# Performance work log

Hardware: AMD Instinct MI355X
Metric: run time of the kernel (lower is better)

The kernel has to match this reference:

```python
import jax, jax.numpy as jnp
import numpy as np

H = 16
NUM_LANDMARKS = 32


def setup_inputs() -> dict:
    key = jax.random.key(0)
    ks = jax.random.split(key, 8)
    B, L, D, hd = 2, 2048, 1024, 64
    x = jax.random.normal(ks[0], (B, L, D), dtype=jnp.float32)
    wscale = 1.0 / np.sqrt(D)
    wq = jax.random.normal(ks[1], (D, D), dtype=jnp.float32) * wscale
    wk = jax.random.normal(ks[2], (D, D), dtype=jnp.float32) * wscale
    wv = jax.random.normal(ks[3], (D, D), dtype=jnp.float32) * wscale
    wo = jax.random.normal(ks[4], (D, D), dtype=jnp.float32) * wscale
    memory_gate = jnp.zeros((1,), dtype=jnp.float32)
    memory_decay = jnp.asarray(2.944, dtype=jnp.float32)
    # standard RoPE angle table: theta_j = 10000^(-2j/hd)
    inv_freq = 1.0 / (10000.0 ** (np.arange(0, hd, 2, dtype=np.float32) / hd))
    ang = np.outer(np.arange(L, dtype=np.float32), inv_freq)  # (L, hd//2)
    freqs_cos = jnp.asarray(np.cos(ang), dtype=jnp.float32)
    freqs_sin = jnp.asarray(np.sin(ang), dtype=jnp.float32)
    # previous-chunk memory: phi features are >= 0, Z accumulates ~NUM_LANDMARKS
    M_old = jax.random.normal(ks[5], (B, H, hd, hd), dtype=jnp.float32) * 0.1
    Z_old = jax.random.uniform(ks[6], (B, H, hd), dtype=jnp.float32) * NUM_LANDMARKS + 1.0
    return {"x": x, "wq": wq, "wk": wk, "wv": wv, "wo": wo,
            "memory_gate": memory_gate, "memory_decay": memory_decay,
            "freqs_cos": freqs_cos, "freqs_sin": freqs_sin,
            "M_old": M_old, "Z_old": Z_old}


def reference(x, wq, wk, wv, wo, memory_gate, memory_decay,
              freqs_cos, freqs_sin, M_old, Z_old):
    B, L, D = x.shape
    hd = D // H

    def proj(w):
        # nn.Linear: x @ W^T, then split heads -> (B, H, L, hd)
        return (x @ w.T).reshape(B, L, H, hd).transpose(0, 2, 1, 3)

    q_base, k_base, v = proj(wq), proj(wk), proj(wv)

    def rope(t):
        # complex multiply on adjacent pairs of the head dim
        tr = t.reshape(B, H, L, hd // 2, 2)
        t0, t1 = tr[..., 0], tr[..., 1]
        cos = freqs_cos[None, None]  # (1,1,L,hd//2)
        sin = freqs_sin[None, None]
        o0 = t0 * cos - t1 * sin
        o1 = t0 * sin + t1 * cos
        return jnp.stack([o0, o1], axis=-1).reshape(B, H, L, hd)

    q_rope, k_rope = rope(q_base), rope(k_base)

    # causal SDPA
    scale = 1.0 / jnp.sqrt(jnp.asarray(hd, dtype=q_rope.dtype))
    scores = jnp.einsum('bhqd,bhkd->bhqk', q_rope, k_rope) * scale
    causal = jnp.tril(jnp.ones((L, L), dtype=bool))
    scores = jnp.where(causal[None, None], scores, jnp.finfo(scores.dtype).min)
    attn = jax.nn.softmax(scores, axis=-1)
    local_out = jnp.einsum('bhqk,bhkd->bhqd', attn, v)

    # linear-attention memory read (uses un-rotated q_base)
    phi_Q = jax.nn.elu(q_base) + 1.0
    num = jnp.einsum('bhld,bhde->bhle', phi_Q, M_old)
    den = jnp.sum(phi_Q * Z_old[:, :, None, :], axis=-1, keepdims=True) + 1e-6
    global_out = num / den
    gate = jax.nn.sigmoid(memory_gate)  # (1,)
    out = local_out + gate * global_out

    # landmark compression: adaptive avg pool == uniform chunk means (L % M == 0)
    def landmarks(t):
        return t.reshape(B, H, NUM_LANDMARKS, L // NUM_LANDMARKS, hd).mean(axis=3)

    phi_K = jax.nn.elu(landmarks(k_base)) + 1.0
    landmark_v = landmarks(v)
    delta_M = jnp.einsum('bhmd,bhme->bhde', phi_K, landmark_v)
    delta_Z = phi_K.sum(axis=-2)

    decay = jax.nn.sigmoid(memory_decay)
    M_new = M_old * decay + delta_M
    Z_new = Z_old * decay + delta_Z

    out = out.transpose(0, 2, 1, 3).reshape(B, L, D)
    y = out @ wo.T
    return y, M_new, Z_new
```

## Files before the change

### kernel.cpp

```cpp
#include <hip/hip_runtime.h>
#include <math.h>

#define NH 16
#define HD 64
#define NB 2
#define LSEQ 2048
#define DM 1024
#define NLM 32

#define OUT_M 4194304
#define OUT_Z 4325376

typedef unsigned short u16;
typedef short bf16x8 __attribute__((ext_vector_type(8)));
typedef float f32x16 __attribute__((ext_vector_type(16)));
typedef unsigned short u16x4 __attribute__((ext_vector_type(4)));

__device__ __forceinline__ float sigmoidf_(float x) { return 1.0f / (1.0f + __expf(-x)); }
__device__ __forceinline__ float phif_(float x) { return x > 0.0f ? x + 1.0f : __expf(x); }

__device__ __forceinline__ u16 f2b(float f) {
    union { float f; unsigned u; } v; v.f = f;
    unsigned r = v.u + 0x7FFFu + ((v.u >> 16) & 1u);
    return (u16)(r >> 16);
}
__device__ __forceinline__ float b2f(u16 b) {
    union { unsigned u; float f; } v; v.u = ((unsigned)b) << 16; return v.f;
}
__device__ __forceinline__ int cvtpkbf(float lo, float hi2) {
    int r;
    asm("v_cvt_pk_bf16_f32 %0, %1, %2" : "=v"(r) : "v"(lo), "v"(hi2));
    return r;
}
__device__ __forceinline__ void gload16(const u16* g, u16* l) {
    __builtin_amdgcn_global_load_lds(
        (const __attribute__((address_space(1))) void*)g,
        (__attribute__((address_space(3))) void*)l, 16, 0, 0);
}

__global__ __launch_bounds__(256) void cvt_all(
    const float* __restrict__ x, const float* __restrict__ wq,
    const float* __restrict__ wk, const float* __restrict__ wv,
    const float* __restrict__ wo, u16* __restrict__ dst) {
    size_t i = ((size_t)blockIdx.x * 256 + threadIdx.x) * 8;
    const float* src;
    size_t off;
    if (i < 4194304)      { src = x;  off = i; }
    else if (i < 5242880) { src = wq; off = i - 4194304; }
    else if (i < 6291456) { src = wk; off = i - 5242880; }
    else if (i < 7340032) { src = wv; off = i - 6291456; }
    else                  { src = wo; off = i - 7340032; }
    float4 a = *(const float4*)(src + off);
    float4 b = *(const float4*)(src + off + 4);
    u16 o[8] = {f2b(a.x), f2b(a.y), f2b(a.z), f2b(a.w),
                f2b(b.x), f2b(b.y), f2b(b.z), f2b(b.w)};
    *(int4*)(dst + i) = *(int4*)o;
}

template <int MODE>
__global__ __launch_bounds__(256) void gemm_mfma(
    const u16* __restrict__ A, const u16* __restrict__ W,
    float* __restrict__ Cf, u16* __restrict__ qb, u16* __restrict__ qrp,
    u16* __restrict__ kbp, u16* __restrict__ krp, u16* __restrict__ vbp,
    const float* __restrict__ fcos, const float* __restrict__ fsin) {
    __shared__ u16 As[128 * 64];
    __shared__ u16 Ws[128 * 64];
    const int tid = threadIdx.x;
    const int m0 = blockIdx.x * 128;
    const int n0 = blockIdx.y * 128;
    const int w = tid >> 6;
    const int lane = tid & 63;
    const int l31 = lane & 31;
    const int khalf = lane >> 5;
    const int wr0 = (w >> 1) * 64;
    const int wc0 = (w & 1) * 64;

    const u16* Ag = A + (size_t)m0 * DM;
    const u16* Wg = W + (size_t)n0 * DM;

    const int st_uoff[4] = {w * 4096, w * 4096 + 1024, w * 4096 + 2048, w * 4096 + 3072};
    int st_row[4], st_cc[4];
#pragma unroll
    for (int i = 0; i < 4; ++i) {
        const int off = st_uoff[i] + lane * 16;
        st_row[i] = off >> 7;
        st_cc[i] = ((off >> 4) & 7) ^ (st_row[i] & 7);
    }

    f32x16 acc[2][2];
#pragma unroll
    for (int mf = 0; mf < 2; ++mf)
#pragma unroll
        for (int nf = 0; nf < 2; ++nf)
#pragma unroll
            for (int i = 0; i < 16; ++i) acc[mf][nf][i] = 0.f;

    for (int k0 = 0; k0 < DM; k0 += 64) {
        __syncthreads();
#pragma unroll
        for (int i = 0; i < 4; ++i)
            gload16(Ag + (size_t)st_row[i] * DM + k0 + st_cc[i] * 8,
                    (u16*)((char*)As + st_uoff[i]));
#pragma unroll
        for (int i = 0; i < 4; ++i)
            gload16(Wg + (size_t)st_row[i] * DM + k0 + st_cc[i] * 8,
                    (u16*)((char*)Ws + st_uoff[i]));
        __syncthreads();
#pragma unroll
        for (int ko = 0; ko < 4; ++ko) {
            const int cl = ko * 2 + khalf;
            const int ra0 = wr0 + l31, ra1 = wr0 + 32 + l31;
            const int rb0 = wc0 + l31, rb1 = wc0 + 32 + l31;
            bf16x8 af0 = *(const bf16x8*)((char*)As + ra0 * 128 + ((cl ^ (ra0 & 7)) * 16));
            bf16x8 af1 = *(const bf16x8*)((char*)As + ra1 * 128 + ((cl ^ (ra1 & 7)) * 16));
            bf16x8 bf0 = *(const bf16x8*)((char*)Ws + rb0 * 128 + ((cl ^ (rb0 & 7)) * 16));
            bf16x8 bf1 = *(const bf16x8*)((char*)Ws + rb1 * 128 + ((cl ^ (rb1 & 7)) * 16));
            acc[0][0] = __builtin_amdgcn_mfma_f32_32x32x16_bf16(af0, bf0, acc[0][0], 0, 0, 0);
            acc[0][1] = __builtin_amdgcn_mfma_f32_32x32x16_bf16(af0, bf1, acc[0][1], 0, 0, 0);
            acc[1][0] = __builtin_amdgcn_mfma_f32_32x32x16_bf16(af1, bf0, acc[1][0], 0, 0, 0);
            acc[1][1] = __builtin_amdgcn_mfma_f32_32x32x16_bf16(af1, bf1, acc[1][1], 0, 0, 0);
        }
    }

#pragma unroll
    for (int mf = 0; mf < 2; ++mf) {
#pragma unroll
        for (int nf = 0; nf < 2; ++nf) {
            const int nn = n0 + wc0 + nf * 32 + l31;
#pragma unroll
            for (int reg = 0; reg < 16; ++reg) {
                const int m = m0 + wr0 + mf * 32 + (reg & 3) + 8 * (reg >> 2) + 4 * khalf;
                const float val = acc[mf][nf][reg];
                if (MODE == 1) {
                    Cf[(size_t)m * DM + nn] = val;
                } else {
                    const int b = m >> 11, l = m & (LSEQ - 1);
                    const int mat = nn >> 10;
                    const int n = nn & 1023;
                    const int h = n >> 6, d = n & 63;
                    const size_t hs = (((size_t)(b * NH + h)) * LSEQ + l) * HD + d;
                    const float p = __shfl_xor(val, 1);
                    if (mat == 2) {
                        vbp[hs] = f2b(val);
                    } else {
                        u16* bs = mat ? kbp : qb;
                        u16* rs = mat ? krp : qrp;
                        bs[hs] = f2b(val);
                        const float c = fcos[l * 32 + (d >> 1)];
                        const float s = fsin[l * 32 + (d >> 1)];
                        float o = (d & 1) ? (p * s + val * c) : (val * c - p * s);
                        if (mat == 0) o *= 0.125f;
                        rs[hs] = f2b(o);
                    }
                }
            }
        }
    }
}

__global__ __launch_bounds__(256) void landmarks(
    const u16* __restrict__ kbase, const u16* __restrict__ vbase,
    float* __restrict__ lkq, float* __restrict__ lvq) {
    __shared__ float redk[4][HD];
    __shared__ float redv[4][HD];
    const int bh = blockIdx.x >> 5;
    const int m = blockIdx.x & 31;
    const int tid = threadIdx.x;
    const int ls = tid >> 6;
    const int d = tid & 63;
    const u16* kb = kbase + ((size_t)bh * LSEQ + m * 64) * HD;
    const u16* vb = vbase + ((size_t)bh * LSEQ + m * 64) * HD;
    float sk = 0.f, sv = 0.f;
    for (int l = ls; l < 64; l += 4) {
        sk += b2f(kb[(size_t)l * HD + d]);
        sv += b2f(vb[(size_t)l * HD + d]);
    }
    redk[ls][d] = sk;
    redv[ls][d] = sv;
    __syncthreads();
    if (tid < 64) {
        float mk = (redk[0][d] + redk[1][d] + redk[2][d] + redk[3][d]) * (1.0f / 64.0f);
        float mv = (redv[0][d] + redv[1][d] + redv[2][d] + redv[3][d]) * (1.0f / 64.0f);
        lkq[((size_t)bh * NLM + m) * HD + d] = phif_(mk);
        lvq[((size_t)bh * NLM + m) * HD + d] = mv;
    }
}

__global__ __launch_bounds__(256) void mem_update(
    const float* __restrict__ lkq, const float* __restrict__ lvq,
    const float* __restrict__ M_old, const float* __restrict__ Z_old,
    const float* __restrict__ decay_p, float* __restrict__ out) {
    __shared__ float lk[NLM][HD];
    __shared__ float lv[NLM][HD];
    const int bh = blockIdx.x;
    const int tid = threadIdx.x;
    const float decay = sigmoidf_(decay_p[0]);
#pragma unroll
    for (int i = 0; i < 8; ++i) {
        int idx = tid + 256 * i;
        lk[idx >> 6][idx & 63] = lkq[(size_t)bh * (NLM * HD) + idx];
        lv[idx >> 6][idx & 63] = lvq[(size_t)bh * (NLM * HD) + idx];
    }
    __syncthreads();
    const size_t mo = (size_t)bh * HD * HD;
#pragma unroll
    for (int p = 0; p < 16; ++p) {
        int idx = tid + 256 * p;
        int dd = idx >> 6, e = idx & 63;
        float s = 0.f;
#pragma unroll
        for (int m = 0; m < NLM; ++m) s = fmaf(lk[m][dd], lv[m][e], s);
        out[OUT_M + mo + idx] = M_old[mo + idx] * decay + s;
    }
    if (tid < 64) {
        float s = 0.f;
#pragma unroll
        for (int m = 0; m < NLM; ++m) s += lk[m][tid];
        out[OUT_Z + (size_t)bh * HD + tid] = Z_old[(size_t)bh * HD + tid] * decay + s;
    }
}

__global__ __launch_bounds__(256) void combine(
    const u16* __restrict__ qbase, const float* __restrict__ att,
    const float* __restrict__ M_old, const float* __restrict__ Z_old,
    const float* __restrict__ gate_p, u16* __restrict__ ctxb) {
    __shared__ float phiQ[64][68];
    __shared__ float Ms[64][64];
    __shared__ float Zs[64];
    const int l0 = blockIdx.x * 64;
    const int bh = blockIdx.y;
    const int b = bh >> 4, h = bh & 15;
    const int tid = threadIdx.x;
    const float gate = sigmoidf_(gate_p[0]);

    {
        const int r = tid >> 2, c0 = (tid & 3) << 4;
        const float* Mo = M_old + (size_t)bh * HD * HD + (size_t)r * HD + c0;
#pragma unroll
        for (int i = 0; i < 4; ++i)
            *reinterpret_cast<float4*>(&Ms[r][c0 + 4 * i]) =
                *reinterpret_cast<const float4*>(Mo + 4 * i);
        if (tid < 64) Zs[tid] = Z_old[(size_t)bh * HD + tid];
        const u16* q = qbase + ((size_t)bh * LSEQ + l0 + r) * HD + c0;
#pragma unroll
        for (int i = 0; i < 4; ++i) {
            u16x4 q4 = *(const u16x4*)(q + 4 * i);
            phiQ[r][c0 + 4 * i + 0] = phif_(b2f(q4[0]));
            phiQ[r][c0 + 4 * i + 1] = phif_(b2f(q4[1]));
            phiQ[r][c0 + 4 * i + 2] = phif_(b2f(q4[2]));
            phiQ[r][c0 + 4 * i + 3] = phif_(b2f(q4[3]));
        }
    }
    __syncthreads();

    const int lr = tid >> 2, sub = tid & 3, e0 = sub << 4;
    float den = 0.f;
#pragma unroll
    for (int i = 0; i < 16; ++i) den = fmaf(phiQ[lr][e0 + i], Zs[e0 + i], den);
    den += __shfl_xor(den, 1);
    den += __shfl_xor(den, 2);
    den += 1e-6f;

    float acc[16] = {};
    for (int dd = 0; dd < 64; ++dd) {
        const float pq = phiQ[lr][dd];
#pragma unroll
        for (int i = 0; i < 16; ++i) acc[i] = fmaf(pq, Ms[dd][e0 + i], acc[i]);
    }
    const float g = gate / den;
    const size_t rowoff = ((size_t)b * LSEQ + l0 + lr) * DM + h * HD + e0;
    const float* ap = att + rowoff;
    u16 o[16];
#pragma unroll
    for (int i = 0; i < 4; ++i) {
        float4 a4 = *(const float4*)(ap + 4 * i);
        o[4 * i + 0] = f2b(a4.x + g * acc[4 * i + 0]);
        o[4 * i + 1] = f2b(a4.y + g * acc[4 * i + 1]);
        o[4 * i + 2] = f2b(a4.z + g * acc[4 * i + 2]);
        o[4 * i + 3] = f2b(a4.w + g * acc[4 * i + 3]);
    }
    *(int4*)(ctxb + rowoff) = *(int4*)o;
    *(int4*)(ctxb + rowoff + 8) = *(int4*)(o + 8);
}

__global__ __launch_bounds__(256) void flash_mfma(
    const u16* __restrict__ qr, const u16* __restrict__ kr,
    const u16* __restrict__ vv, float* __restrict__ att) {
    __shared__ int4 smem4[2048];
    char* lds = (char*)smem4;

    const int bid = blockIdx.x;
    const int bx = (bid < 256) ? (15 - (bid >> 5)) : ((bid - 256) >> 5);
    const int bh = bid & 31;
    const int q0 = bx * 128;
    const int tid = threadIdx.x;
    const int w = tid >> 6;
    const int lane = tid & 63;
    const int hi = lane >> 5;
    const int l31 = lane & 31;
    const int qw0 = q0 + w * 32;
    const int tdiag = qw0 >> 6;
    const int nt = 2 * bx + 2;
    const size_t base_bh = (size_t)bh * (LSEQ * HD);

#pragma unroll
    for (int i = 0; i < 4; ++i) {
        int u = tid + 256 * i;
        int row = u >> 3, c = u & 7;
        int4 val = *(const int4*)(qr + base_bh + (size_t)(q0 + row) * HD + c * 8);
        *(int4*)(lds + 16384 + row * 128 + ((c ^ (row & 7)) * 16)) = val;
    }

    int r_[2], c_[2], skoff_[2], svoff_[2];
#pragma unroll
    for (int j = 0; j < 2; ++j) {
        int u = tid + 256 * j;
        int r = u >> 3, c = u & 7;
        r_[j] = r; c_[j] = c;
        skoff_[j] = r * 128 + ((c ^ (r & 7)) * 16);
        int d0 = c << 3;
        svoff_[j] = (r >> 5) * 4096 + (d0 >> 5) * 2048 + (d0 & 31) * 64
                  + ((((r & 31) >> 3) ^ ((d0 >> 3) & 3)) * 16 + (r & 7) * 2);
    }

    int4 RAk[2], RAv[2], RBk[2], RBv[2];
    auto load_tile = [&](int t, int4* Rk, int4* Rv) {
#pragma unroll
        for (int j = 0; j < 2; ++j) {
            Rk[j] = *(const int4*)(kr + base_bh + (size_t)(t * 64 + r_[j]) * HD + c_[j] * 8);
            Rv[j] = *(const int4*)(vv + base_bh + (size_t)(t * 64 + r_[j]) * HD + c_[j] * 8);
        }
    };
    auto write_tile = [&](int base, int4* Rk, int4* Rv) {
#pragma unroll
        for (int j = 0; j < 2; ++j) {
            *(int4*)(lds + base + skoff_[j]) = Rk[j];
            union { int4 q; u16 h[8]; } uv; uv.q = Rv[j];
            char* vd = lds + base + 8192 + svoff_[j];
#pragma unroll
            for (int e = 0; e < 8; ++e) *(u16*)(vd + e * 64) = uv.h[e];
        }
    };

    load_tile(0, RAk, RAv);
    __syncthreads();

    bf16x8 qf[4];
    {
        const char* qrow = lds + 16384 + ((w << 5) + l31) * 128;
        const int sw = l31 & 7;
#pragma unroll
        for (int ks = 0; ks < 4; ++ks) {
            int c = 2 * ks + hi;
            qf[ks] = *(const bf16x8*)(qrow + ((c ^ sw) * 16));
        }
    }
    write_tile(0, RAk, RAv);
    load_tile(1, RBk, RBv);
    __syncthreads();

    f32x16 accO[2];
#pragma unroll
    for (int mf = 0; mf < 2; ++mf)
#pragma unroll
        for (int i = 0; i < 16; ++i) accO[mf][i] = 0.f;
    float m_run = -INFINITY, l_run = 0.f;
    const int swK = l31 & 7;
    const int vsw = (l31 >> 3) & 3;

    auto compute_tile = [&](int t, int base) {
        const char* Kb = lds + base;
        const char* Vb = lds + base + 8192;
        f32x16 st0, st1;
#pragma unroll
        for (int i = 0; i < 16; ++i) { st0[i] = 0.f; st1[i] = 0.f; }
        __builtin_amdgcn_s_setprio(1);
#pragma unroll
        for (int ks = 0; ks < 4; ++ks) {
            int c = 2 * ks + hi;
            bf16x8 kf0 = *(const bf16x8*)(Kb + l31 * 128 + ((c ^ swK) * 16));
            bf16x8 kf1 = *(const bf16x8*)(Kb + (32 + l31) * 128 + ((c ^ swK) * 16));
            st0 = __builtin_amdgcn_mfma_f32_32x32x16_bf16(kf0, qf[ks], st0, 0, 0, 0);
            st1 = __builtin_amdgcn_mfma_f32_32x32x16_bf16(kf1, qf[ks], st1, 0, 0, 0);
        }
        __builtin_amdgcn_s_setprio(0);
        bf16x8 va[2][2][2];
#pragma unroll
        for (int sub = 0; sub < 2; ++sub)
#pragma unroll
            for (int kb2 = 0; kb2 < 2; ++kb2)
#pragma unroll
                for (int mf = 0; mf < 2; ++mf)
                    va[sub][kb2][mf] = *(const bf16x8*)(
                        Vb + sub * 4096 + mf * 2048 + l31 * 64 + (((kb2 * 2 + hi) ^ vsw) * 16));

        float s[32];
#pragma unroll
        for (int r = 0; r < 16; ++r) { s[r] = st0[r]; s[16 + r] = st1[r]; }
        if (t == tdiag) {
            const int qg = qw0 + l31;
#pragma unroll
            for (int r = 0; r < 32; ++r) {
                int keyg = t * 64 + (r >> 4) * 32 + (r & 3) + 8 * ((r >> 2) & 3) + 4 * hi;
                if (keyg > qg) s[r] = -INFINITY;
            }
        }
        float t16[16];
#pragma unroll
        for (int r = 0; r < 16; ++r) t16[r] = fmaxf(s[r], s[r + 16]);
        float t8[8];
#pragma unroll
        for (int r = 0; r < 8; ++r) t8[r] = fmaxf(t16[r], t16[r + 8]);
        float t4[4];
#pragma unroll
        for (int r = 0; r < 4; ++r) t4[r] = fmaxf(t8[r], t8[r + 4]);
        float pm = fmaxf(fmaxf(t4[0], t4[1]), fmaxf(t4[2], t4[3]));
        pm = fmaxf(pm, __shfl_xor(pm, 32));
        if (!__all(pm - m_run <= 8.f)) {
            const float mn = fmaxf(m_run, pm);
            const float sc = __expf(m_run - mn);
#pragma unroll
            for (int mf = 0; mf < 2; ++mf)
#pragma unroll
                for (int i = 0; i < 16; ++i) accO[mf][i] *= sc;
            l_run *= sc;
            m_run = mn;
        }
        float p[32];
#pragma unroll
        for (int r = 0; r < 32; ++r) p[r] = __expf(s[r] - m_run);
        float a16[16];
#pragma unroll
        for (int r = 0; r < 16; ++r) a16[r] = p[r] + p[r + 16];
        float a8[8];
#pragma unroll
        for (int r = 0; r < 8; ++r) a8[r] = a16[r] + a16[r + 8];
        float a4[4];
#pragma unroll
        for (int r = 0; r < 4; ++r) a4[r] = a8[r] + a8[r + 4];
        float ss = (a4[0] + a4[1]) + (a4[2] + a4[3]);
        ss += __shfl_xor(ss, 32);
        l_run += ss;

        int pk[16];
#pragma unroll
        for (int i = 0; i < 16; ++i) pk[i] = cvtpkbf(p[2 * i], p[2 * i + 1]);
        int xp[16];
#pragma unroll
        for (int i = 0; i < 16; ++i) xp[i] = __shfl_xor(pk[i], 32);
        const bool hib = (hi != 0);
        union { int i[4]; bf16x8 v; } pu[4];
#pragma unroll
        for (int g = 0; g < 4; ++g) {
            const int o = g * 4;
            pu[g].i[0] = hib ? xp[o + 2] : pk[o + 0];
            pu[g].i[1] = hib ? xp[o + 3] : pk[o + 1];
            pu[g].i[2] = hib ? pk[o + 2] : xp[o + 0];
            pu[g].i[3] = hib ? pk[o + 3] : xp[o + 1];
        }
        __builtin_amdgcn_s_setprio(1);
        accO[0] = __builtin_amdgcn_mfma_f32_32x32x16_bf16(va[0][0][0], pu[0].v, accO[0], 0, 0, 0);
        accO[1] = __builtin_amdgcn_mfma_f32_32x32x16_bf16(va[0][0][1], pu[0].v, accO[1], 0, 0, 0);
        accO[0] = __builtin_amdgcn_mfma_f32_32x32x16_bf16(va[0][1][0], pu[1].v, accO[0], 0, 0, 0);
        accO[1] = __builtin_amdgcn_mfma_f32_32x32x16_bf16(va[0][1][1], pu[1].v, accO[1], 0, 0, 0);
        accO[0] = __builtin_amdgcn_mfma_f32_32x32x16_bf16(va[1][0][0], pu[2].v, accO[0], 0, 0, 0);
        accO[1] = __builtin_amdgcn_mfma_f32_32x32x16_bf16(va[1][0][1], pu[2].v, accO[1], 0, 0, 0);
        accO[0] = __builtin_amdgcn_mfma_f32_32x32x16_bf16(va[1][1][0], pu[3].v, accO[0], 0, 0, 0);
        accO[1] = __builtin_amdgcn_mfma_f32_32x32x16_bf16(va[1][1][1], pu[3].v, accO[1], 0, 0, 0);
        __builtin_amdgcn_s_setprio(0);
    };

    for (int t = 0; t < nt; t += 2) {
        write_tile(16384, RBk, RBv);
        if (t + 2 < nt) load_tile(t + 2, RAk, RAv);
        if (t <= tdiag) compute_tile(t, 0);
        __syncthreads();
        if (t + 2 < nt) write_tile(0, RAk, RAv);
        if (t + 3 < nt) load_tile(t + 3, RBk, RBv);
        if (t + 1 <= tdiag) compute_tile(t + 1, 16384);
        __syncthreads();
    }

    const float invl = 1.0f / l_run;
    const int qg = qw0 + l31;
    float* abase = att + ((size_t)(bh >> 4) * LSEQ + qg) * DM + (bh & 15) * HD;
#pragma unroll
    for (int mf = 0; mf < 2; ++mf) {
#pragma unroll
        for (int g = 0; g < 4; ++g) {
            const int d4 = mf * 32 + 8 * g + 4 * hi;
            float4 c4 = make_float4(accO[mf][g * 4 + 0] * invl, accO[mf][g * 4 + 1] * invl,
                                    accO[mf][g * 4 + 2] * invl, accO[mf][g * 4 + 3] * invl);
            *(float4*)(abase + d4) = c4;
        }
    }
}

extern "C" void kernel_launch(void* const* d_in, const int* in_sizes, int n_in,
                              void* d_out, int out_size, void* d_ws, size_t ws_size,
                              hipStream_t stream) {
    const float* x     = (const float*)d_in[0];
    const float* wq    = (const float*)d_in[1];
    const float* wk    = (const float*)d_in[2];
    const float* wv    = (const float*)d_in[3];
    const float* wo    = (const float*)d_in[4];
    const float* gate  = (const float*)d_in[5];
    const float* decay = (const float*)d_in[6];
    const float* fcos  = (const float*)d_in[7];
    const float* fsin  = (const float*)d_in[8];
    const float* M_old = (const float*)d_in[9];
    const float* Z_old = (const float*)d_in[10];
    float* out = (float*)d_out;

    u16* xb     = (u16*)d_ws;
    u16* wqkv   = xb + 4194304;
    u16* wob    = wqkv + 3145728;
    u16* q_rope = wob + 1048576;
    u16* q_base = q_rope + 4194304;
    u16* k_rope = q_base + 4194304;
    u16* k_base = k_rope + 4194304;
    u16* v      = k_base + 4194304;
    float* att  = (float*)(v + 4194304);
    float* lkq  = (float*)wqkv;
    float* lvq  = lkq + 65536;
    u16* ctxb   = xb;

    dim3 bb(256);
    cvt_all<<<dim3(4096), bb, 0, stream>>>(x, wq, wk, wv, wo, xb);

    gemm_mfma<4><<<dim3(32, 24), bb, 0, stream>>>(xb, wqkv, nullptr, q_base, q_rope,
                                                  k_base, k_rope, v, fcos, fsin);

    landmarks<<<dim3(NB * NH * NLM), bb, 0, stream>>>(k_base, v, lkq, lvq);
    mem_update<<<dim3(NB * NH), bb, 0, stream>>>(lkq, lvq, M_old, Z_old, decay, out);
    flash_mfma<<<dim3(512), bb, 0, stream>>>(q_rope, k_rope, v, att);
    combine<<<dim3(LSEQ / 64, NB * NH), bb, 0, stream>>>(q_base, att, M_old, Z_old, gate, ctxb);

    gemm_mfma<1><<<dim3(32, 8), bb, 0, stream>>>(ctxb, wob, out, nullptr, nullptr,
                                                 nullptr, nullptr, nullptr, nullptr, nullptr);
}
```

Before: 181.1 us.

## Pair complementary query tiles per 512-thread block and use exp2 softmax

The flash attention kernel now runs 256 blocks of 512 threads. Each block handles a long query tile and its mirrored short query tile for the same head, so both tiles share one K/V tile load from LDS. LDS use doubles and each thread stages one K/V chunk instead of two. Separately, log2(e) is folded into the q scale so the softmax can use exp2f instead of __expf, and the rescale threshold is adjusted to match. The wave group with the short tile presumably idles on tiles past its diagonal, and the doubled LDS footprint may reduce occupancy.

```diff
diff --git a/kernel.cpp b/kernel.cpp
--- a/kernel.cpp
+++ b/kernel.cpp
@@ -149,7 +149,7 @@
                         const float c = fcos[l * 32 + (d >> 1)];
                         const float s = fsin[l * 32 + (d >> 1)];
                         float o = (d & 1) ? (p * s + val * c) : (val * c - p * s);
-                        if (mat == 0) o *= 0.125f;
+                        if (mat == 0) o *= 0.18033688f;
                         rs[hs] = f2b(o);
                     }
                 }
@@ -283,63 +283,56 @@
     *(int4*)(ctxb + rowoff + 8) = *(int4*)(o + 8);
 }
 
-__global__ __launch_bounds__(256) void flash_mfma(
+__global__ __launch_bounds__(512) void flash_mfma(
     const u16* __restrict__ qr, const u16* __restrict__ kr,
     const u16* __restrict__ vv, float* __restrict__ att) {
-    __shared__ int4 smem4[2048];
+    __shared__ int4 smem4[4096];
     char* lds = (char*)smem4;
 
     const int bid = blockIdx.x;
-    const int bx = (bid < 256) ? (15 - (bid >> 5)) : ((bid - 256) >> 5);
     const int bh = bid & 31;
-    const int q0 = bx * 128;
+    const int pr = bid >> 5;
+    const int qa = 15 - pr;
+    const int qb = pr;
     const int tid = threadIdx.x;
     const int w = tid >> 6;
+    const int wgrp = w >> 2;
+    const int wsub = w & 3;
     const int lane = tid & 63;
     const int hi = lane >> 5;
     const int l31 = lane & 31;
-    const int qw0 = q0 + w * 32;
+    const int qtile = wgrp ? qb : qa;
+    const int qw0 = qtile * 128 + wsub * 32;
     const int tdiag = qw0 >> 6;
-    const int nt = 2 * bx + 2;
+    const int nt = 2 * qa + 2;
     const size_t base_bh = (size_t)bh * (LSEQ * HD);
 
 #pragma unroll
     for (int i = 0; i < 4; ++i) {
-        int u = tid + 256 * i;
+        int u = tid + 512 * i;
         int row = u >> 3, c = u & 7;
-        int4 val = *(const int4*)(qr + base_bh + (size_t)(q0 + row) * HD + c * 8);
-        *(int4*)(lds + 16384 + row * 128 + ((c ^ (row & 7)) * 16)) = val;
-    }
-
-    int r_[2], c_[2], skoff_[2], svoff_[2];
-#pragma unroll
-    for (int j = 0; j < 2; ++j) {
-        int u = tid + 256 * j;
-        int r = u >> 3, c = u & 7;
-        r_[j] = r; c_[j] = c;
-        skoff_[j] = r * 128 + ((c ^ (r & 7)) * 16);
-        int d0 = c << 3;
-        svoff_[j] = (r >> 5) * 4096 + (d0 >> 5) * 2048 + (d0 & 31) * 64
-                  + ((((r & 31) >> 3) ^ ((d0 >> 3) & 3)) * 16 + (r & 7) * 2);
-    }
-
-    int4 RAk[2], RAv[2], RBk[2], RBv[2];
-    auto load_tile = [&](int t, int4* Rk, int4* Rv) {
-#pragma unroll
-        for (int j = 0; j < 2; ++j) {
-            Rk[j] = *(const int4*)(kr + base_bh + (size_t)(t * 64 + r_[j]) * HD + c_[j] * 8);
-            Rv[j] = *(const int4*)(vv + base_bh + (size_t)(t * 64 + r_[j]) * HD + c_[j] * 8);
-        }
+        int grow = (row < 128) ? (qa * 128 + row) : (qb * 128 + (row & 127));
+        int4 val = *(const int4*)(qr + base_bh + (size_t)grow * HD + c * 8);
+        *(int4*)(lds + 32768 + row * 128 + ((c ^ (row & 7)) * 16)) = val;
+    }
+
+    const int sr = tid >> 3, sc = tid & 7;
+    const int skoff = sr * 128 + ((sc ^ (sr & 7)) * 16);
+    const int sd0 = sc << 3;
+    const int svoff = (sr >> 5) * 4096 + (sd0 >> 5) * 2048 + (sd0 & 31) * 64
+                    + ((((sr & 31) >> 3) ^ ((sd0 >> 3) & 3)) * 16 + (sr & 7) * 2);
+
+    int4 RAk, RAv, RBk, RBv;
+    auto load_tile = [&](int t, int4& Rk, int4& Rv) {
+        Rk = *(const int4*)(kr + base_bh + (size_t)(t * 64 + sr) * HD + sc * 8);
+        Rv = *(const int4*)(vv + base_bh + (size_t)(t * 64 + sr) * HD + sc * 8);
     };
-    auto write_tile = [&](int base, int4* Rk, int4* Rv) {
-#pragma unroll
-        for (int j = 0; j < 2; ++j) {
-            *(int4*)(lds + base + skoff_[j]) = Rk[j];
-            union { int4 q; u16 h[8]; } uv; uv.q = Rv[j];
-            char* vd = lds + base + 8192 + svoff_[j];
-#pragma unroll
-            for (int e = 0; e < 8; ++e) *(u16*)(vd + e * 64) = uv.h[e];
-        }
+    auto write_tile = [&](int base, int4& Rk, int4& Rv) {
+        *(int4*)(lds + base + skoff) = Rk;
+        union { int4 q; u16 h[8]; } uv; uv.q = Rv;
+        char* vd = lds + base + 8192 + svoff;
+#pragma unroll
+        for (int e = 0; e < 8; ++e) *(u16*)(vd + e * 64) = uv.h[e];
     };
 
     load_tile(0, RAk, RAv);
@@ -347,12 +340,13 @@
 
     bf16x8 qf[4];
     {
-        const char* qrow = lds + 16384 + ((w << 5) + l31) * 128;
+        const int qrow = wgrp * 128 + wsub * 32 + l31;
+        const char* qp = lds + 32768 + qrow * 128;
         const int sw = l31 & 7;
 #pragma unroll
         for (int ks = 0; ks < 4; ++ks) {
             int c = 2 * ks + hi;
-            qf[ks] = *(const bf16x8*)(qrow + ((c ^ sw) * 16));
+            qf[ks] = *(const bf16x8*)(qp + ((c ^ sw) * 16));
         }
     }
     write_tile(0, RAk, RAv);
@@ -416,9 +410,9 @@
         for (int r = 0; r < 4; ++r) t4[r] = fmaxf(t8[r], t8[r + 4]);
         float pm = fmaxf(fmaxf(t4[0], t4[1]), fmaxf(t4[2], t4[3]));
         pm = fmaxf(pm, __shfl_xor(pm, 32));
-        if (!__all(pm - m_run <= 8.f)) {
+        if (!__all(pm - m_run <= 11.5416f)) {
             const float mn = fmaxf(m_run, pm);
-            const float sc = __expf(m_run - mn);
+            const float sc = exp2f(m_run - mn);
 #pragma unroll
             for (int mf = 0; mf < 2; ++mf)
 #pragma unroll
@@ -428,7 +422,7 @@
         }
         float p[32];
 #pragma unroll
-        for (int r = 0; r < 32; ++r) p[r] = __expf(s[r] - m_run);
+        for (int r = 0; r < 32; ++r) p[r] = exp2f(s[r] - m_run);
         float a16[16];
 #pragma unroll
         for (int r = 0; r < 16; ++r) a16[r] = p[r] + p[r + 16];
@@ -533,7 +527,7 @@
 
     landmarks<<<dim3(NB * NH * NLM), bb, 0, stream>>>(k_base, v, lkq, lvq);
     mem_update<<<dim3(NB * NH), bb, 0, stream>>>(lkq, lvq, M_old, Z_old, decay, out);
-    flash_mfma<<<dim3(512), bb, 0, stream>>>(q_rope, k_rope, v, att);
+    flash_mfma<<<dim3(256), dim3(512), 0, stream>>>(q_rope, k_rope, v, att);
     combine<<<dim3(LSEQ / 64, NB * NH), bb, 0, stream>>>(q_base, att, M_old, Z_old, gate, ctxb);
 
     gemm_mfma<1><<<dim3(32, 8), bb, 0, stream>>>(ctxb, wob, out, nullptr, nullptr,
```

Result: faster. 177.1 us (-2.2%).

## Split causal attention KV range in two and merge partials in combine

Applied to the files above, without the earlier changes.

The flash attention kernel now launches twice as many blocks, with each query tile's key range split into two halves. Each half writes a bf16 partial output plus its running max and sum, and the combine kernel merges the two partials with log-sum-exp weights. The change also folds log2(e) into the q scale so the softmax can use exp2f, and swaps the fp32 attention buffer for bf16 partials. This aims to fix load imbalance and too few blocks on the long diagonal tiles, at the cost of extra partial traffic and bf16 rounding of the partials. The LDS allocation grows to 48KB, which may reduce occupancy.

```diff
diff --git a/kernel.cpp b/kernel.cpp
--- a/kernel.cpp
+++ b/kernel.cpp
@@ -15,6 +15,7 @@
 typedef short bf16x8 __attribute__((ext_vector_type(8)));
 typedef float f32x16 __attribute__((ext_vector_type(16)));
 typedef unsigned short u16x4 __attribute__((ext_vector_type(4)));
+typedef unsigned long long ull;
 
 __device__ __forceinline__ float sigmoidf_(float x) { return 1.0f / (1.0f + __expf(-x)); }
 __device__ __forceinline__ float phif_(float x) { return x > 0.0f ? x + 1.0f : __expf(x); }
@@ -26,6 +27,9 @@
 }
 __device__ __forceinline__ float b2f(u16 b) {
     union { unsigned u; float f; } v; v.u = ((unsigned)b) << 16; return v.f;
+}
+__device__ __forceinline__ ull pack4(float a, float b, float c, float d) {
+    return (ull)f2b(a) | ((ull)f2b(b) << 16) | ((ull)f2b(c) << 32) | ((ull)f2b(d) << 48);
 }
 __device__ __forceinline__ int cvtpkbf(float lo, float hi2) {
     int r;
@@ -149,7 +153,7 @@
                         const float c = fcos[l * 32 + (d >> 1)];
                         const float s = fsin[l * 32 + (d >> 1)];
                         float o = (d & 1) ? (p * s + val * c) : (val * c - p * s);
-                        if (mat == 0) o *= 0.125f;
+                        if (mat == 0) o *= 0.18033688f;
                         rs[hs] = f2b(o);
                     }
                 }
@@ -221,9 +225,10 @@
 }
 
 __global__ __launch_bounds__(256) void combine(
-    const u16* __restrict__ qbase, const float* __restrict__ att,
-    const float* __restrict__ M_old, const float* __restrict__ Z_old,
-    const float* __restrict__ gate_p, u16* __restrict__ ctxb) {
+    const u16* __restrict__ qbase, const u16* __restrict__ opart,
+    const float2* __restrict__ ml, const float* __restrict__ M_old,
+    const float* __restrict__ Z_old, const float* __restrict__ gate_p,
+    u16* __restrict__ ctxb) {
     __shared__ float phiQ[64][68];
     __shared__ float Ms[64][64];
     __shared__ float Zs[64];
@@ -268,16 +273,37 @@
         for (int i = 0; i < 16; ++i) acc[i] = fmaf(pq, Ms[dd][e0 + i], acc[i]);
     }
     const float g = gate / den;
-    const size_t rowoff = ((size_t)b * LSEQ + l0 + lr) * DM + h * HD + e0;
-    const float* ap = att + rowoff;
+
+    const int row = l0 + lr;
+    const float2 m0 = ml[bh * LSEQ + row];
+    const float2 m1 = ml[32 * LSEQ + bh * LSEQ + row];
+    const float mm = fmaxf(m0.x, m1.x);
+    float a0 = exp2f(m0.x - mm) * m0.y;
+    float a1 = exp2f(m1.x - mm) * m1.y;
+    const float inv = 1.0f / (a0 + a1);
+    a0 *= inv; a1 *= inv;
+
+    const size_t prow = ((size_t)bh * LSEQ + row) * HD + e0;
+    const u16* o0p = opart + prow;
+    const u16* o1p = opart + 4194304 + prow;
+    int4 o0a = *(const int4*)o0p;
+    int4 o0b = *(const int4*)(o0p + 8);
+    int4 o1a = *(const int4*)o1p;
+    int4 o1b = *(const int4*)(o1p + 8);
+    const u16* u0a = (const u16*)&o0a; const u16* u0b = (const u16*)&o0b;
+    const u16* u1a = (const u16*)&o1a; const u16* u1b = (const u16*)&o1b;
+
+    const size_t rowoff = ((size_t)b * LSEQ + row) * DM + h * HD + e0;
     u16 o[16];
 #pragma unroll
-    for (int i = 0; i < 4; ++i) {
-        float4 a4 = *(const float4*)(ap + 4 * i);
-        o[4 * i + 0] = f2b(a4.x + g * acc[4 * i + 0]);
-        o[4 * i + 1] = f2b(a4.y + g * acc[4 * i + 1]);
-        o[4 * i + 2] = f2b(a4.z + g * acc[4 * i + 2]);
-        o[4 * i + 3] = f2b(a4.w + g * acc[4 * i + 3]);
+    for (int i = 0; i < 8; ++i) {
+        float att = a0 * b2f(u0a[i]) + a1 * b2f(u1a[i]);
+        o[i] = f2b(att + g * acc[i]);
+    }
+#pragma unroll
+    for (int i = 0; i < 8; ++i) {
+        float att = a0 * b2f(u0b[i]) + a1 * b2f(u1b[i]);
+        o[8 + i] = f2b(att + g * acc[8 + i]);
     }
     *(int4*)(ctxb + rowoff) = *(int4*)o;
     *(int4*)(ctxb + rowoff + 8) = *(int4*)(o + 8);
@@ -285,14 +311,16 @@
 
 __global__ __launch_bounds__(256) void flash_mfma(
     const u16* __restrict__ qr, const u16* __restrict__ kr,
-    const u16* __restrict__ vv, float* __restrict__ att) {
-    __shared__ int4 smem4[2048];
+    const u16* __restrict__ vv, u16* __restrict__ opart,
+    float2* __restrict__ ml) {
+    __shared__ int4 smem4[3072];
     char* lds = (char*)smem4;
 
     const int bid = blockIdx.x;
-    const int bx = (bid < 256) ? (15 - (bid >> 5)) : ((bid - 256) >> 5);
+    const int qt = 15 - (bid >> 6);
+    const int half = (bid >> 5) & 1;
     const int bh = bid & 31;
-    const int q0 = bx * 128;
+    const int q0 = qt * 128;
     const int tid = threadIdx.x;
     const int w = tid >> 6;
     const int lane = tid & 63;
@@ -300,7 +328,8 @@
     const int l31 = lane & 31;
     const int qw0 = q0 + w * 32;
     const int tdiag = qw0 >> 6;
-    const int nt = 2 * bx + 2;
+    const int t0 = half ? (qt + 1) : 0;
+    const int t1 = half ? (2 * qt + 2) : (qt + 1);
     const size_t base_bh = (size_t)bh * (LSEQ * HD);
 
 #pragma unroll
@@ -308,7 +337,7 @@
         int u = tid + 256 * i;
         int row = u >> 3, c = u & 7;
         int4 val = *(const int4*)(qr + base_bh + (size_t)(q0 + row) * HD + c * 8);
-        *(int4*)(lds + 16384 + row * 128 + ((c ^ (row & 7)) * 16)) = val;
+        *(int4*)(lds + 32768 + row * 128 + ((c ^ (row & 7)) * 16)) = val;
     }
 
     int r_[2], c_[2], skoff_[2], svoff_[2];
@@ -342,21 +371,21 @@
         }
     };
 
-    load_tile(0, RAk, RAv);
+    load_tile(t0, RAk, RAv);
     __syncthreads();
 
     bf16x8 qf[4];
     {
-        const char* qrow = lds + 16384 + ((w << 5) + l31) * 128;
+        const char* qp = lds + 32768 + ((w << 5) + l31) * 128;
         const int sw = l31 & 7;
 #pragma unroll
         for (int ks = 0; ks < 4; ++ks) {
             int c = 2 * ks + hi;
-            qf[ks] = *(const bf16x8*)(qrow + ((c ^ sw) * 16));
+            qf[ks] = *(const bf16x8*)(qp + ((c ^ sw) * 16));
         }
     }
     write_tile(0, RAk, RAv);
-    load_tile(1, RBk, RBv);
+    if (t0 + 1 < t1) load_tile(t0 + 1, RBk, RBv);
     __syncthreads();
 
     f32x16 accO[2];
@@ -416,9 +445,9 @@
         for (int r = 0; r < 4; ++r) t4[r] = fmaxf(t8[r], t8[r + 4]);
         float pm = fmaxf(fmaxf(t4[0], t4[1]), fmaxf(t4[2], t4[3]));
         pm = fmaxf(pm, __shfl_xor(pm, 32));
-        if (!__all(pm - m_run <= 8.f)) {
+        if (!__all(pm - m_run <= 11.5416f)) {
             const float mn = fmaxf(m_run, pm);
-            const float sc = __expf(m_run - mn);
+            const float sc = exp2f(m_run - mn);
 #pragma unroll
             for (int mf = 0; mf < 2; ++mf)
 #pragma unroll
@@ -428,7 +457,7 @@
         }
         float p[32];
 #pragma unroll
-        for (int r = 0; r < 32; ++r) p[r] = __expf(s[r] - m_run);
+        for (int r = 0; r < 32; ++r) p[r] = exp2f(s[r] - m_run);
         float a16[16];
 #pragma unroll
         for (int r = 0; r < 16; ++r) a16[r] = p[r] + p[r + 16];
@@ -470,30 +499,33 @@
         __builtin_amdgcn_s_setprio(0);
     };
 
-    for (int t = 0; t < nt; t += 2) {
-        write_tile(16384, RBk, RBv);
-        if (t + 2 < nt) load_tile(t + 2, RAk, RAv);
+    for (int t = t0; t < t1; t += 2) {
+        if (t + 1 < t1) write_tile(16384, RBk, RBv);
+        if (t + 2 < t1) load_tile(t + 2, RAk, RAv);
         if (t <= tdiag) compute_tile(t, 0);
         __syncthreads();
-        if (t + 2 < nt) write_tile(0, RAk, RAv);
-        if (t + 3 < nt) load_tile(t + 3, RBk, RBv);
-        if (t + 1 <= tdiag) compute_tile(t + 1, 16384);
+        if (t + 2 < t1) write_tile(0, RAk, RAv);
+        if (t + 3 < t1) load_tile(t + 3, RBk, RBv);
+        if (t + 1 < t1 && t + 1 <= tdiag) compute_tile(t + 1, 16384);
         __syncthreads();
     }
 
-    const float invl = 1.0f / l_run;
+    const float invl = (l_run > 0.f) ? (1.0f / l_run) : 0.f;
     const int qg = qw0 + l31;
-    float* abase = att + ((size_t)(bh >> 4) * LSEQ + qg) * DM + (bh & 15) * HD;
+    u16* obase = opart + (half ? 4194304 : 0) + ((size_t)bh * LSEQ + qg) * HD;
 #pragma unroll
     for (int mf = 0; mf < 2; ++mf) {
 #pragma unroll
         for (int g = 0; g < 4; ++g) {
             const int d4 = mf * 32 + 8 * g + 4 * hi;
-            float4 c4 = make_float4(accO[mf][g * 4 + 0] * invl, accO[mf][g * 4 + 1] * invl,
-                                    accO[mf][g * 4 + 2] * invl, accO[mf][g * 4 + 3] * invl);
-            *(float4*)(abase + d4) = c4;
-        }
-    }
+            *(ull*)(obase + d4) = pack4(accO[mf][g * 4 + 0] * invl,
+                                        accO[mf][g * 4 + 1] * invl,
+                                        accO[mf][g * 4 + 2] * invl,
+                                        accO[mf][g * 4 + 3] * invl);
+        }
+    }
+    if (hi == 0)
+        ml[(half ? 32 * LSEQ : 0) + bh * LSEQ + qg] = make_float2(m_run, l_run);
 }
 
 extern "C" void kernel_launch(void* const* d_in, const int* in_sizes, int n_in,
@@ -520,9 +552,11 @@
     u16* k_rope = q_base + 4194304;
     u16* k_base = k_rope + 4194304;
     u16* v      = k_base + 4194304;
-    float* att  = (float*)(v + 4194304);
-    float* lkq  = (float*)wqkv;
-    float* lvq  = lkq + 65536;
+    u16* opart  = v + 4194304;
+    float* wsf  = (float*)wqkv;
+    float* lkq  = wsf;
+    float* lvq  = wsf + 65536;
+    float2* ml  = (float2*)(wsf + 131072);
     u16* ctxb   = xb;
 
     dim3 bb(256);
@@ -533,8 +567,9 @@
 
     landmarks<<<dim3(NB * NH * NLM), bb, 0, stream>>>(k_base, v, lkq, lvq);
     mem_update<<<dim3(NB * NH), bb, 0, stream>>>(lkq, lvq, M_old, Z_old, decay, out);
-    flash_mfma<<<dim3(512), bb, 0, stream>>>(q_rope, k_rope, v, att);
-    combine<<<dim3(LSEQ / 64, NB * NH), bb, 0, stream>>>(q_base, att, M_old, Z_old, gate, ctxb);
+    flash_mfma<<<dim3(1024), bb, 0, stream>>>(q_rope, k_rope, v, opart, ml);
+    combine<<<dim3(LSEQ / 64, NB * NH), bb, 0, stream>>>(q_base, opart, ml, M_old,
+                                                         Z_old, gate, ctxb);
 
     gemm_mfma<1><<<dim3(32, 8), bb, 0, stream>>>(ctxb, wob, out, nullptr, nullptr,
                                                  nullptr, nullptr, nullptr, nullptr, nullptr);
```

New measurement: 173.6 us. 1.04x faster.
